# Kernel tuning notes

Measured on AMD Instinct MI355X. Metric: run time of the kernel, lower is better.

Reference implementation:

```python
import jax, jax.numpy as jnp
import numpy as np

NK, NQ, D = 8192, 8192, 64


def setup_inputs() -> dict:
    key = jax.random.key(0)
    k1, k2, k3, k4 = jax.random.split(key, 4)
    K = jax.random.normal(k1, (NK, D), dtype=jnp.float32)
    V = jax.random.normal(k2, (NK, D), dtype=jnp.float32)
    Q = jax.random.normal(k3, (NQ, D), dtype=jnp.float32)
    m = jax.random.normal(k4, (NQ, NK), dtype=jnp.float32)  # additive edge/mask data
    return {"K": K, "V": V, "Q": Q, "m": m}


def reference(K, V, Q, m):
    d = Q.shape[-1]
    scale = 1.0 / jnp.sqrt(jnp.asarray(d, dtype=Q.dtype))
    # affinity: scaled dot product + additive m (edge information / mask)
    QKt = jnp.einsum("qd,kd->qk", Q, K) * scale + m  # [NQ, NK]
    # norm: softmax over keys
    QKt_n = jax.nn.softmax(QKt, axis=-1)
    return QKt_n @ V  # [NQ, D]
```

## Files before the change

kernel.cpp:

```cpp
#include <hip/hip_runtime.h>

#define NKK 8192
#define NQQ 8192
#define DDIM 64

typedef __attribute__((ext_vector_type(8))) short short8;
typedef __attribute__((ext_vector_type(4))) float f32x4;
typedef __attribute__((ext_vector_type(2))) unsigned int u32x2;

static __device__ __forceinline__ unsigned short f2b(float x) {
  unsigned int u = __builtin_bit_cast(unsigned int, x);
  unsigned int r = (u + 0x7fffu + ((u >> 16) & 1u)) >> 16;
  return (unsigned short)r;
}
static __device__ __forceinline__ unsigned int pk2(float a, float b) {
  return (unsigned int)f2b(a) | ((unsigned int)f2b(b) << 16);
}

__global__ __launch_bounds__(256) void prep_kernel(
    const float* __restrict__ K, const float* __restrict__ V, const float* __restrict__ Q,
    unsigned short* __restrict__ Kb, unsigned short* __restrict__ Qb, unsigned short* __restrict__ Vtb) {
  __shared__ unsigned short vt[64][72];
  const int b = blockIdx.x, t = threadIdx.x;
  const size_t base = (size_t)b * 4096;
#pragma unroll
  for (int i = 0; i < 4; ++i) {
    size_t idx = base + (size_t)i * 1024 + (size_t)t * 4;
    float4 kv = *(const float4*)(K + idx);
    float4 qv = *(const float4*)(Q + idx);
    ushort4 ko, qo;
    ko.x = f2b(kv.x); ko.y = f2b(kv.y); ko.z = f2b(kv.z); ko.w = f2b(kv.w);
    qo.x = f2b(qv.x); qo.y = f2b(qv.y); qo.z = f2b(qv.z); qo.w = f2b(qv.w);
    *(ushort4*)(Kb + idx) = ko;
    *(ushort4*)(Qb + idx) = qo;
  }
  const int r0 = b * 64;
#pragma unroll
  for (int i = 0; i < 4; ++i) {
    int kl = (t >> 4) + i * 16;
    int c4 = (t & 15) * 4;
    float4 v = *(const float4*)(V + (size_t)(r0 + kl) * 64 + c4);
    vt[c4 + 0][kl] = f2b(v.x);
    vt[c4 + 1][kl] = f2b(v.y);
    vt[c4 + 2][kl] = f2b(v.z);
    vt[c4 + 3][kl] = f2b(v.w);
  }
  __syncthreads();
  {
    int d = t >> 2, kc = (t & 3) * 16;
    uint4 a0 = *(const uint4*)(&vt[d][kc]);
    uint4 a1 = *(const uint4*)(&vt[d][kc + 8]);
    *(uint4*)(Vtb + (size_t)d * NKK + r0 + kc) = a0;
    *(uint4*)(Vtb + (size_t)d * NKK + r0 + kc + 8) = a1;
  }
}

__global__ __launch_bounds__(512, 4) void attn_kernel(
    const float* __restrict__ mg, const unsigned short* __restrict__ Kb,
    const unsigned short* __restrict__ Qb, const unsigned short* __restrict__ Vtb,
    float* __restrict__ out) {
  __shared__ unsigned short Pl[8][16][40];
  __shared__ float accslot[4][4][4][64];
  __shared__ float lslot[4][64];

  const int tid = threadIdx.x;
  const int wid = tid >> 6;
  const int lane = tid & 63;
  const int c = lane & 15;
  const int g = lane >> 4;
  const int q0 = blockIdx.x * 16;

  const float LOG2E = 1.4426950408889634f;
  const float C1 = 0.125f * LOG2E;
  const float MM = -8.0f * LOG2E;

  short8 qf[2];
#pragma unroll
  for (int dh = 0; dh < 2; ++dh)
    qf[dh] = __builtin_bit_cast(
        short8, *(const uint4*)(Qb + (size_t)(q0 + c) * 64 + dh * 32 + 8 * g));

  f32x4 acc[4];
#pragma unroll
  for (int dt = 0; dt < 4; ++dt) acc[dt] = f32x4{0.f, 0.f, 0.f, 0.f};
  float lsum = 0.f;

  const float* mrow = mg + (size_t)(q0 + c) * NKK + 4 * g;

  f32x4 mA[2], mB[2];

  auto loadM = [&](int t, f32x4 (&mb)[2]) {
    const float* p = mrow + (unsigned)((wid + 8 * t) * 32);
    mb[0] = *(const f32x4*)(p);
    mb[1] = *(const f32x4*)(p + 16);
  };

  auto computeTile = [&](int t, const f32x4 (&mb)[2]) {
    const int k0 = (wid + 8 * t) * 32;
    short8 kf[4];
#pragma unroll
    for (int kb = 0; kb < 2; ++kb)
#pragma unroll
      for (int dh = 0; dh < 2; ++dh)
        kf[kb * 2 + dh] = __builtin_bit_cast(
            short8, *(const uint4*)(Kb + (size_t)(k0 + kb * 16 + c) * 64 + dh * 32 + 8 * g));
    short8 vf[4];
#pragma unroll
    for (int dt = 0; dt < 4; ++dt)
      vf[dt] = __builtin_bit_cast(
          short8, *(const uint4*)(Vtb + (size_t)(dt * 16 + c) * NKK + k0 + 8 * g));

#pragma unroll
    for (int kb = 0; kb < 2; ++kb) {
      f32x4 z = f32x4{0.f, 0.f, 0.f, 0.f};
      z = __builtin_amdgcn_mfma_f32_16x16x32_bf16(kf[kb * 2 + 0], qf[0], z, 0, 0, 0);
      z = __builtin_amdgcn_mfma_f32_16x16x32_bf16(kf[kb * 2 + 1], qf[1], z, 0, 0, 0);
      float p[4];
#pragma unroll
      for (int i = 0; i < 4; ++i) {
        float e = __builtin_fmaf(z[i], C1, __builtin_fmaf(mb[kb][i], LOG2E, MM));
        p[i] = __builtin_amdgcn_exp2f(e);
        lsum += p[i];
      }
      u32x2 w;
      w[0] = pk2(p[0], p[1]);
      w[1] = pk2(p[2], p[3]);
      *(u32x2*)(&Pl[wid][c][kb * 16 + 4 * g]) = w;
    }
    short8 pa = __builtin_bit_cast(short8, *(const uint4*)(&Pl[wid][c][8 * g]));
#pragma unroll
    for (int dt = 0; dt < 4; ++dt)
      acc[dt] = __builtin_amdgcn_mfma_f32_16x16x32_bf16(pa, vf[dt], acc[dt], 0, 0, 0);
  };

  loadM(0, mA);
  loadM(1, mB);
  for (int t = 0; t < 32; t += 2) {
    computeTile(t, mA);
    if (t + 2 < 32) loadM(t + 2, mA);
    computeTile(t + 1, mB);
    if (t + 3 < 32) loadM(t + 3, mB);
  }

  lsum += __shfl_xor(lsum, 16);
  lsum += __shfl_xor(lsum, 32);

  auto writeSlot = [&](int slot) {
#pragma unroll
    for (int dt = 0; dt < 4; ++dt)
#pragma unroll
      for (int i = 0; i < 4; ++i) accslot[slot][dt][i][lane] = acc[dt][i];
    lslot[slot][lane] = lsum;
  };
  auto addSlot = [&](int slot) {
#pragma unroll
    for (int dt = 0; dt < 4; ++dt)
#pragma unroll
      for (int i = 0; i < 4; ++i) acc[dt][i] += accslot[slot][dt][i][lane];
    lsum += lslot[slot][lane];
  };

  if (wid >= 4) writeSlot(wid - 4);
  __syncthreads();
  if (wid < 4) addSlot(wid);
  __syncthreads();
  if (wid == 2 || wid == 3) writeSlot(wid - 2);
  __syncthreads();
  if (wid < 2) addSlot(wid);
  __syncthreads();
  if (wid == 1) writeSlot(0);
  __syncthreads();
  if (wid == 0) {
    addSlot(0);
#pragma unroll
    for (int i = 0; i < 4; ++i) {
      float rs = __shfl(lsum, 4 * g + i);
      float rl = 1.0f / rs;
      const int q = q0 + 4 * g + i;
#pragma unroll
      for (int dt = 0; dt < 4; ++dt)
        out[(size_t)q * 64 + dt * 16 + c] = acc[dt][i] * rl;
    }
  }
}

extern "C" void kernel_launch(void* const* d_in, const int* in_sizes, int n_in,
                              void* d_out, int out_size, void* d_ws, size_t ws_size,
                              hipStream_t stream) {
  (void)in_sizes; (void)n_in; (void)out_size; (void)ws_size;
  const float* K = (const float*)d_in[0];
  const float* V = (const float*)d_in[1];
  const float* Q = (const float*)d_in[2];
  const float* mg = (const float*)d_in[3];
  float* out = (float*)d_out;

  unsigned short* Kb = (unsigned short*)d_ws;
  unsigned short* Qb = Kb + (size_t)NKK * DDIM;
  unsigned short* Vtb = Qb + (size_t)NQQ * DDIM;

  prep_kernel<<<128, 256, 0, stream>>>(K, V, Q, Kb, Qb, Vtb);
  attn_kernel<<<512, 512, 0, stream>>>(mg, Kb, Qb, Vtb, out);
}
```

Measured before the change: 454.6 us.

## Stage mask tiles into LDS with async global_load_lds double buffering

Stops each lane loading its mask values straight from global memory in registers. The block now cooperatively streams a 16x256 mask tile into double-buffered, XOR-swizzled LDS using global_load_lds, prefetching the next tile while the current one is computed. Tile ownership changes so all 8 waves share one 256-key chunk per iteration, which adds a __syncthreads per iteration. Shared memory grows to about 42 KB per block, which may limit occupancy under launch_bounds(512,4).

```diff
diff --git a/kernel.cpp b/kernel.cpp
--- a/kernel.cpp
+++ b/kernel.cpp
@@ -59,9 +59,7 @@
     const float* __restrict__ mg, const unsigned short* __restrict__ Kb,
     const unsigned short* __restrict__ Qb, const unsigned short* __restrict__ Vtb,
     float* __restrict__ out) {
-  __shared__ unsigned short Pl[8][16][40];
-  __shared__ float accslot[4][4][4][64];
-  __shared__ float lslot[4][64];
+  __shared__ __align__(16) char smem[43008];
 
   const int tid = threadIdx.x;
   const int wid = tid >> 6;
@@ -85,30 +83,53 @@
   for (int dt = 0; dt < 4; ++dt) acc[dt] = f32x4{0.f, 0.f, 0.f, 0.f};
   float lsum = 0.f;
 
-  const float* mrow = mg + (size_t)(q0 + c) * NKK + 4 * g;
-
-  f32x4 mA[2], mB[2];
-
-  auto loadM = [&](int t, f32x4 (&mb)[2]) {
-    const float* p = mrow + (unsigned)((wid + 8 * t) * 32);
-    mb[0] = *(const f32x4*)(p);
-    mb[1] = *(const f32x4*)(p + 16);
+  unsigned short* Pw = (unsigned short*)(smem + 32768) + wid * 640;
+  const unsigned short* Pr = Pw + c * 40 + 8 * g;
+
+  auto stageM = [&](int t, int buf) {
+    const unsigned o = (unsigned)tid * 16u;
+#pragma unroll
+    for (int h = 0; h < 2; ++h) {
+      unsigned oo = o + (unsigned)h * 8192u;
+      unsigned row = oo >> 10;
+      unsigned cb = (oo & 1023u) ^ ((row & 7u) << 4);
+      const float* src = mg + (size_t)(q0 + (int)row) * NKK + (unsigned)t * 256u + (cb >> 2);
+      char* dst = smem + buf * 16384 + oo;
+      __builtin_amdgcn_global_load_lds(
+          (const __attribute__((address_space(1))) void*)src,
+          (__attribute__((address_space(3))) void*)dst, 16, 0, 0);
+    }
   };
 
-  auto computeTile = [&](int t, const f32x4 (&mb)[2]) {
-    const int k0 = (wid + 8 * t) * 32;
-    short8 kf[4];
+  stageM(0, 0);
+  __syncthreads();
+
+  const unsigned sw = ((unsigned)(c & 7)) << 4;
+
+  for (int t = 0; t < 32; ++t) {
+    const int cur = t & 1;
+    const int k0 = t * 256 + wid * 32;
+
+    short8 kf[4], vf[4];
 #pragma unroll
     for (int kb = 0; kb < 2; ++kb)
 #pragma unroll
       for (int dh = 0; dh < 2; ++dh)
         kf[kb * 2 + dh] = __builtin_bit_cast(
             short8, *(const uint4*)(Kb + (size_t)(k0 + kb * 16 + c) * 64 + dh * 32 + 8 * g));
-    short8 vf[4];
 #pragma unroll
     for (int dt = 0; dt < 4; ++dt)
       vf[dt] = __builtin_bit_cast(
           short8, *(const uint4*)(Vtb + (size_t)(dt * 16 + c) * NKK + k0 + 8 * g));
+    __builtin_amdgcn_sched_barrier(0);
+
+    if (t + 1 < 32) stageM(t + 1, cur ^ 1);
+    __builtin_amdgcn_sched_barrier(0);
+
+    const char* mrow = smem + cur * 16384 + c * 1024;
+    f32x4 mb[2];
+    mb[0] = *(const f32x4*)(mrow + (((unsigned)(wid * 128 + g * 16)) ^ sw));
+    mb[1] = *(const f32x4*)(mrow + (((unsigned)(wid * 128 + g * 16 + 64)) ^ sw));
 
 #pragma unroll
     for (int kb = 0; kb < 2; ++kb) {
@@ -125,39 +146,37 @@
       u32x2 w;
       w[0] = pk2(p[0], p[1]);
       w[1] = pk2(p[2], p[3]);
-      *(u32x2*)(&Pl[wid][c][kb * 16 + 4 * g]) = w;
+      *(u32x2*)(Pw + c * 40 + kb * 16 + 4 * g) = w;
     }
-    short8 pa = __builtin_bit_cast(short8, *(const uint4*)(&Pl[wid][c][8 * g]));
+    short8 pa = __builtin_bit_cast(short8, *(const uint4*)(Pr));
 #pragma unroll
     for (int dt = 0; dt < 4; ++dt)
       acc[dt] = __builtin_amdgcn_mfma_f32_16x16x32_bf16(pa, vf[dt], acc[dt], 0, 0, 0);
-  };
-
-  loadM(0, mA);
-  loadM(1, mB);
-  for (int t = 0; t < 32; t += 2) {
-    computeTile(t, mA);
-    if (t + 2 < 32) loadM(t + 2, mA);
-    computeTile(t + 1, mB);
-    if (t + 3 < 32) loadM(t + 3, mB);
+
+    __syncthreads();
   }
 
   lsum += __shfl_xor(lsum, 16);
   lsum += __shfl_xor(lsum, 32);
 
+  float* accs = (float*)smem;
+  float* lsl = (float*)(smem + 16384);
+
   auto writeSlot = [&](int slot) {
-#pragma unroll
-    for (int dt = 0; dt < 4; ++dt)
-#pragma unroll
-      for (int i = 0; i < 4; ++i) accslot[slot][dt][i][lane] = acc[dt][i];
-    lslot[slot][lane] = lsum;
+    float* s = accs + slot * 1024;
+#pragma unroll
+    for (int dt = 0; dt < 4; ++dt)
+#pragma unroll
+      for (int i = 0; i < 4; ++i) s[(dt * 4 + i) * 64 + lane] = acc[dt][i];
+    lsl[slot * 64 + lane] = lsum;
   };
   auto addSlot = [&](int slot) {
-#pragma unroll
-    for (int dt = 0; dt < 4; ++dt)
-#pragma unroll
-      for (int i = 0; i < 4; ++i) acc[dt][i] += accslot[slot][dt][i][lane];
-    lsum += lslot[slot][lane];
+    const float* s = accs + slot * 1024;
+#pragma unroll
+    for (int dt = 0; dt < 4; ++dt)
+#pragma unroll
+      for (int i = 0; i < 4; ++i) acc[dt][i] += s[(dt * 4 + i) * 64 + lane];
+    lsum += lsl[slot * 64 + lane];
   };
 
   if (wid >= 4) writeSlot(wid - 4);
```

Result: faster. 413.4 us (-9.1%).
